# Kernel optimization log

Hardware: AMD Instinct MI355X
Metric: run time of the kernel (lower is better)

## Reference

```python
import jax, jax.numpy as jnp
import numpy as np

INF = 1.0e6
SIGMA = 1.0
RADIUS = 2.5
M, N, H, K, C_IN, C_OUT = 50000, 50000, 32, 15, 128, 128
EXTENT = 10.0  # spatial extent of the random point cloud


def setup_inputs() -> dict:
    key = jax.random.key(0)
    k1, k2, k3, k4, k5, k6 = jax.random.split(key, 6)
    q_pts = jax.random.uniform(k1, (M, 3), dtype=jnp.float32) * EXTENT
    s_pts = jax.random.uniform(k2, (N, 3), dtype=jnp.float32) * EXTENT
    s_feats = jax.random.normal(k3, (N, C_IN), dtype=jnp.float32)
    neighb_inds = jax.random.randint(k4, (M, H), 0, N, dtype=jnp.int64)
    # kernel points: random points inside sphere of given radius (stand-in for load_kernels)
    kp = jax.random.normal(k5, (K, 3), dtype=jnp.float32)
    kp = kp / jnp.linalg.norm(kp, axis=1, keepdims=True) * (RADIUS * 0.66)
    kernel_points = kp.at[0].set(0.0)  # fixed center point
    # kaiming-uniform-like init
    bound = 1.0 / np.sqrt(C_IN)
    weights = jax.random.uniform(k6, (K, C_IN, C_OUT), dtype=jnp.float32,
                                 minval=-bound, maxval=bound)
    return {"q_pts": q_pts, "s_pts": s_pts, "s_feats": s_feats,
            "neighb_inds": neighb_inds, "kernel_points": kernel_points,
            "weights": weights}


def reference(q_pts, s_pts, s_feats, neighb_inds, kernel_points, weights):
    # pad support points with a far-away point so out-of-range indices get zero influence
    s_pts_pad = jnp.concatenate([s_pts, jnp.full((1, 3), INF, s_pts.dtype)], axis=0)
    neighbors = s_pts_pad[neighb_inds] - q_pts[:, None, :]          # (M, H, 3)
    diffs = neighbors[:, :, None, :] - kernel_points[None, None]    # (M, H, K, 3)
    sq_dist = jnp.sum(diffs * diffs, axis=-1)                       # (M, H, K)
    # linear influence, clipped at 0 (no_grad in torch -> stop_gradient here)
    w = jnp.clip(1.0 - jnp.sqrt(sq_dist) / SIGMA, 0.0)              # (M, H, K)
    neighbor_weights = jax.lax.stop_gradient(jnp.swapaxes(w, 1, 2)) # (M, K, H)
    # gather neighbor features (padded with a zero row)
    feats_pad = jnp.concatenate([s_feats, jnp.zeros((1, s_feats.shape[1]), s_feats.dtype)], axis=0)
    neighbor_feats = feats_pad[neighb_inds]                         # (M, H, C_in)
    weighted_feats = jnp.matmul(neighbor_weights, neighbor_feats)   # (M, K, C_in)
    return jnp.einsum('mkc,kcd->md', weighted_feats, weights)       # (M, C_out)
```

## Files before the change

### kernel.cpp

```cpp
#include <hip/hip_runtime.h>

#define M_Q 50000
#define N_S 50000
#define H_N 32
#define K_P 15
#define C_IN 128
#define C_OUT 128

#define G_QB 64
#define G_NT 256
#define NB_GEO ((M_Q + G_QB - 1) / G_QB)
#define LCAP 64

#define WTF_SLOTS (K_P * 8 * 4 * 64)
#define NB_WCVT (WTF_SLOTS / 256)

#define NB_ZERO 1024

#define ENT 128
#define SUBT (ENT / 16)
#define CAPK 12288
#define K2_TILES (CAPK / ENT)

#define WS_CNT_OFF 0
#define WS_WTF_OFF 256
#define WS_WTF_BYTES (WTF_SLOTS * 16)
#define WS_BKT_OFF (WS_WTF_OFF + WS_WTF_BYTES)
#define WS_BKT_BYTES (K_P * CAPK * 8)
#define WS_NEED (WS_BKT_OFF + WS_BKT_BYTES)

typedef __attribute__((ext_vector_type(8))) short s8v;
typedef __attribute__((ext_vector_type(4))) float f4v;
typedef __attribute__((ext_vector_type(4))) float fl4;
typedef __attribute__((ext_vector_type(4))) unsigned u4v;

static __device__ __forceinline__ unsigned f2bf_bits(float x) {
    union { float f; unsigned u; } v; v.f = x;
    return (v.u + 0x7fffu + ((v.u >> 16) & 1u)) >> 16;
}
static __device__ __forceinline__ unsigned pack_bf16(float a, float b) {
    return f2bf_bits(a) | (f2bf_bits(b) << 16);
}

template <typename IT>
__global__ __launch_bounds__(G_NT) void k1_geom(
    const float* __restrict__ q_pts,
    const float* __restrict__ s_pts,
    const IT* __restrict__ inds,
    const float* __restrict__ kp,
    const float* __restrict__ W,
    unsigned* __restrict__ ws_u,
    float* __restrict__ out)
{
    const int b = blockIdx.x;
    const int t = threadIdx.x;

    if (b >= NB_GEO) {
        if (b >= NB_GEO + NB_WCVT) {
            const int zb = b - NB_GEO - NB_WCVT;
            fl4* o4 = (fl4*)out;
            const fl4 z = {0.0f, 0.0f, 0.0f, 0.0f};
            for (int i = zb * G_NT + t; i < M_Q * C_OUT / 4; i += NB_ZERO * G_NT)
                o4[i] = z;
            return;
        }
        const int i = (b - NB_GEO) * 256 + t;
        if (i < WTF_SLOTS) {
            const int lane = i & 63;
            const int kk = (i >> 6) & 3;
            const int col = (i >> 8) & 7;
            const int k = i >> 11;
            const int d = col * 16 + (lane & 15);
            const int c0 = kk * 32 + (lane >> 4) * 8;
            unsigned short* dst =
                (unsigned short*)((char*)ws_u + WS_WTF_OFF) + (size_t)i * 8;
            u4v g;
            unsigned short* gs = (unsigned short*)&g;
            #pragma unroll
            for (int j = 0; j < 8; ++j)
                gs[j] = (unsigned short)f2bf_bits(W[((size_t)k * 128 + c0 + j) * 128 + d]);
            *(u4v*)dst = g;
        }
        return;
    }

    __shared__ float s_kp[K_P * 3];
    __shared__ float s_q[G_QB * 3];
    __shared__ int s_lcnt[K_P];
    __shared__ uint2 s_le[K_P][LCAP];
    __shared__ int s_gb[K_P], s_gc[K_P];

    const int qbase = b * G_QB;
    if (t < K_P * 3) s_kp[t] = kp[t];
    if (t < K_P) s_lcnt[t] = 0;
    if (t < G_QB * 3) {
        int g = qbase * 3 + t;
        s_q[t] = (g < M_Q * 3) ? q_pts[g] : 0.0f;
    }
    __syncthreads();

    #pragma unroll
    for (int it = 0; it < 8; ++it) {
        const int task = it * G_NT + t;
        const int q = task >> 5, h = task & 31;
        const int qg = qbase + q;
        if (qg < M_Q) {
            long long idx = (long long)inds[(size_t)qg * H_N + h];
            if ((unsigned long long)idx < (unsigned long long)N_S) {
                const int i32 = (int)idx;
                const float rx = s_pts[i32 * 3 + 0] - s_q[q * 3 + 0];
                const float ry = s_pts[i32 * 3 + 1] - s_q[q * 3 + 1];
                const float rz = s_pts[i32 * 3 + 2] - s_q[q * 3 + 2];
                #pragma unroll
                for (int k = 0; k < K_P; ++k) {
                    const float dx = rx - s_kp[k * 3 + 0];
                    const float dy = ry - s_kp[k * 3 + 1];
                    const float dz = rz - s_kp[k * 3 + 2];
                    const float d2 = dx * dx + dy * dy + dz * dz;
                    if (d2 < 1.0f) {
                        const float wgt = 1.0f - sqrtf(d2);
                        const int pos = atomicAdd(&s_lcnt[k], 1);
                        if (pos < LCAP)
                            s_le[k][pos] = make_uint2(((unsigned)qg << 16) | (unsigned)i32,
                                                      __float_as_uint(wgt));
                    }
                }
            }
        }
    }
    __syncthreads();

    if (t < K_P) {
        const int cl = min(s_lcnt[t], LCAP);
        const int base = (int)atomicAdd(&ws_u[t], (unsigned)cl);
        s_gb[t] = base;
        const int avail = CAPK - base;
        s_gc[t] = max(0, min(cl, avail));
    }
    __syncthreads();

    uint2* bkt = (uint2*)((char*)ws_u + WS_BKT_OFF);
    #pragma unroll
    for (int k = 0; k < K_P; ++k) {
        if (t < s_gc[k])
            bkt[(size_t)k * CAPK + s_gb[k] + t] = s_le[k][t];
    }
}

__global__ __launch_bounds__(256, 3) void k2_gemm(
    const float* __restrict__ s_feats,
    const unsigned* __restrict__ ws_u,
    float* __restrict__ out)
{
    const int k = blockIdx.x;
    const int base = blockIdx.y * ENT;
    const int cnt = min((int)ws_u[k], CAPK);
    int n_e = cnt - base;
    if (n_e <= 0) return;
    if (n_e > ENT) n_e = ENT;

    __shared__ unsigned short s_A[SUBT * 4 * 64 * 8];
    __shared__ unsigned s_mi[ENT];

    const int t = threadIdx.x;
    const int lane = t & 63;
    const int w = t >> 6;
    const int quad = lane >> 4, l15 = lane & 15;

    const unsigned short* wk =
        (const unsigned short*)((const char*)ws_u + WS_WTF_OFF) + (size_t)k * 2048 * 8;
    s8v bf[2][4];
    #pragma unroll
    for (int nc = 0; nc < 2; ++nc)
        #pragma unroll
        for (int kk = 0; kk < 4; ++kk)
            bf[nc][kk] = *(const s8v*)(wk +
                (size_t)((((w * 2 + nc) * 4) + kk) * 64 + lane) * 8);

    const int e = t >> 1, half = t & 1;
    {
        const int sub = e >> 4, l15e = e & 15;
        if (e < n_e) {
            const uint2* bkt = (const uint2*)((const char*)ws_u + WS_BKT_OFF)
                               + (size_t)k * CAPK + base;
            const uint2 be = bkt[e];
            const unsigned mi = be.x;
            const float wgt = __uint_as_float(be.y);
            if (half == 0) s_mi[e] = mi;
            const float* fr = s_feats + (size_t)(mi & 0xffffu) * C_IN + half * 64;
            #pragma unroll
            for (int j = 0; j < 4; ++j) {
                const fl4 fa = *(const fl4*)(fr + j * 16);
                const fl4 fb = *(const fl4*)(fr + j * 16 + 4);
                const fl4 fc = *(const fl4*)(fr + j * 16 + 8);
                const fl4 fd = *(const fl4*)(fr + j * 16 + 12);
                u4v g0, g1;
                g0[0] = pack_bf16(wgt * fa.x, wgt * fa.y);
                g0[1] = pack_bf16(wgt * fa.z, wgt * fa.w);
                g0[2] = pack_bf16(wgt * fb.x, wgt * fb.y);
                g0[3] = pack_bf16(wgt * fb.z, wgt * fb.w);
                g1[0] = pack_bf16(wgt * fc.x, wgt * fc.y);
                g1[1] = pack_bf16(wgt * fc.z, wgt * fc.w);
                g1[2] = pack_bf16(wgt * fd.x, wgt * fd.y);
                g1[3] = pack_bf16(wgt * fd.z, wgt * fd.w);
                const int cs = half * 64 + j * 16;
                const int kk = cs >> 5;
                const int qd = (cs >> 3) & 3;
                *(u4v*)&s_A[(size_t)(((sub * 4 + kk) * 64) + qd * 16 + l15e) * 8] = g0;
                *(u4v*)&s_A[(size_t)(((sub * 4 + kk) * 64) + (qd + 1) * 16 + l15e) * 8] = g1;
            }
        } else {
            if (half == 0) s_mi[e] = 0xffffffffu;
            const u4v z = {0u, 0u, 0u, 0u};
            #pragma unroll
            for (int j = 0; j < 4; ++j) {
                const int cs = half * 64 + j * 16;
                const int kk = cs >> 5;
                const int qd = (cs >> 3) & 3;
                *(u4v*)&s_A[(size_t)(((sub * 4 + kk) * 64) + qd * 16 + l15e) * 8] = z;
                *(u4v*)&s_A[(size_t)(((sub * 4 + kk) * 64) + (qd + 1) * 16 + l15e) * 8] = z;
            }
        }
    }
    __syncthreads();

    const f4v zf = {0.0f, 0.0f, 0.0f, 0.0f};
    f4v acc[SUBT][2];
    #pragma unroll
    for (int s = 0; s < SUBT; ++s) { acc[s][0] = zf; acc[s][1] = zf; }

    #pragma unroll
    for (int s = 0; s < SUBT; ++s) {
        s8v af[4];
        #pragma unroll
        for (int kk = 0; kk < 4; ++kk)
            af[kk] = *(const s8v*)&s_A[(size_t)((s * 4 + kk) * 64 + lane) * 8];
        #pragma unroll
        for (int nc = 0; nc < 2; ++nc)
            #pragma unroll
            for (int kk = 0; kk < 4; ++kk)
                acc[s][nc] = __builtin_amdgcn_mfma_f32_16x16x32_bf16(
                    af[kk], bf[nc][kk], acc[s][nc], 0, 0, 0);
    }

    #pragma unroll
    for (int s = 0; s < SUBT; ++s) {
        #pragma unroll
        for (int r = 0; r < 4; ++r) {
            const unsigned mi = s_mi[s * 16 + quad * 4 + r];
            const unsigned m = mi >> 16;
            if (m < M_Q) {
                float* op = out + (size_t)m * C_OUT + w * 32 + l15;
                atomicAdd(op,      acc[s][0][r]);
                atomicAdd(op + 16, acc[s][1][r]);
            }
        }
    }
}

template <typename IT>
__global__ __launch_bounds__(128, 8) void kpconv_v1(
    const float* __restrict__ q_pts, const float* __restrict__ s_pts,
    const float* __restrict__ s_feats, const IT* __restrict__ neighb_inds,
    const float* __restrict__ kernel_points, const float* __restrict__ weights,
    float* __restrict__ out)
{
    __shared__ float s_kp[K_P * 3];
    __shared__ float s_w[K_P][H_N];
    __shared__ int s_idx[H_N];
    __shared__ unsigned s_hmask, s_kmask;
    __shared__ float s_wf[K_P][C_IN];
    const int m = blockIdx.x, tid = threadIdx.x;
    if (tid < K_P * 3) s_kp[tid] = kernel_points[tid];
    if (tid == 0) { s_hmask = 0u; s_kmask = 0u; }
    __syncthreads();
    if (tid < H_N) {
        long long idx = (long long)neighb_inds[(size_t)m * H_N + tid];
        const float qx = q_pts[m * 3], qy = q_pts[m * 3 + 1], qz = q_pts[m * 3 + 2];
        float rx, ry, rz; int idx32;
        if ((unsigned long long)idx < (unsigned long long)N_S) {
            idx32 = (int)idx;
            rx = s_pts[idx32 * 3] - qx; ry = s_pts[idx32 * 3 + 1] - qy; rz = s_pts[idx32 * 3 + 2] - qz;
        } else { idx32 = 0; rx = ry = rz = 1.0e6f; }
        s_idx[tid] = idx32;
        unsigned kmask = 0u;
        #pragma unroll
        for (int k = 0; k < K_P; ++k) {
            const float dx = rx - s_kp[k * 3], dy = ry - s_kp[k * 3 + 1], dz = rz - s_kp[k * 3 + 2];
            const float w = fmaxf(1.0f - sqrtf(dx * dx + dy * dy + dz * dz), 0.0f);
            s_w[k][tid] = w;
            if (w > 0.0f) kmask |= (1u << k);
        }
        if (kmask) { atomicOr(&s_hmask, 1u << tid); atomicOr(&s_kmask, kmask); }
    }
    __syncthreads();
    const unsigned hmask = s_hmask, kmask = s_kmask;
    float wf[K_P];
    #pragma unroll
    for (int k = 0; k < K_P; ++k) wf[k] = 0.0f;
    unsigned hmv = hmask;
    while (hmv) {
        const int h = __builtin_ctz(hmv); hmv &= hmv - 1;
        const float f = s_feats[(size_t)s_idx[h] * C_IN + tid];
        #pragma unroll
        for (int k = 0; k < K_P; ++k) wf[k] = fmaf(s_w[k][h], f, wf[k]);
    }
    #pragma unroll
    for (int k = 0; k < K_P; ++k) s_wf[k][tid] = wf[k];
    __syncthreads();
    float a = 0.0f;
    unsigned km = kmask;
    while (km) {
        const int k = __builtin_ctz(km); km &= km - 1;
        const float* Wk = weights + (size_t)k * C_IN * C_OUT + tid;
        #pragma unroll 8
        for (int c = 0; c < C_IN; ++c) a = fmaf(s_wf[k][c], Wk[(size_t)c * C_OUT], a);
    }
    out[(size_t)m * C_OUT + tid] = a;
}

extern "C" void kernel_launch(void* const* d_in, const int* in_sizes, int n_in,
                              void* d_out, int out_size, void* d_ws, size_t ws_size,
                              hipStream_t stream) {
    const float* q_pts         = (const float*)d_in[0];
    const float* s_pts         = (const float*)d_in[1];
    const float* s_feats       = (const float*)d_in[2];
    const float* kernel_points = (const float*)d_in[4];
    const float* weights       = (const float*)d_in[5];
    float* out = (float*)d_out;
    const bool i64 = (in_sizes[3] == 2 * M_Q * H_N);

    if (ws_size < (size_t)WS_NEED) {
        dim3 grid(M_Q), block(128);
        if (i64)
            kpconv_v1<long long><<<grid, block, 0, stream>>>(
                q_pts, s_pts, s_feats, (const long long*)d_in[3], kernel_points, weights, out);
        else
            kpconv_v1<int><<<grid, block, 0, stream>>>(
                q_pts, s_pts, s_feats, (const int*)d_in[3], kernel_points, weights, out);
        return;
    }

    unsigned* ws_u = (unsigned*)d_ws;
    hipMemsetAsync(d_ws, 0, 64, stream);

    dim3 g1(NB_GEO + NB_WCVT + NB_ZERO), b1(G_NT);
    if (i64)
        k1_geom<long long><<<g1, b1, 0, stream>>>(
            q_pts, s_pts, (const long long*)d_in[3], kernel_points, weights, ws_u, out);
    else
        k1_geom<int><<<g1, b1, 0, stream>>>(
            q_pts, s_pts, (const int*)d_in[3], kernel_points, weights, ws_u, out);

    dim3 g2(K_P, K2_TILES), b2(256);
    k2_gemm<<<g2, b2, 0, stream>>>(s_feats, ws_u, out);
}
```

Baseline: 159.1 us.

## Fuse geometry and per-kernel-point MFMA into one kernel with shared-memory accumulation

```diff
diff --git a/kernel.cpp b/kernel.cpp
--- a/kernel.cpp
+++ b/kernel.cpp
@@ -11,23 +11,11 @@
 #define G_NT 256
 #define NB_GEO ((M_Q + G_QB - 1) / G_QB)
 #define LCAP 64
+#define ACC_STRIDE 132
 
 #define WTF_SLOTS (K_P * 8 * 4 * 64)
 #define NB_WCVT (WTF_SLOTS / 256)
-
-#define NB_ZERO 1024
-
-#define ENT 128
-#define SUBT (ENT / 16)
-#define CAPK 12288
-#define K2_TILES (CAPK / ENT)
-
-#define WS_CNT_OFF 0
-#define WS_WTF_OFF 256
-#define WS_WTF_BYTES (WTF_SLOTS * 16)
-#define WS_BKT_OFF (WS_WTF_OFF + WS_WTF_BYTES)
-#define WS_BKT_BYTES (K_P * CAPK * 8)
-#define WS_NEED (WS_BKT_OFF + WS_BKT_BYTES)
+#define WS_NEED (WTF_SLOTS * 16)
 
 typedef __attribute__((ext_vector_type(8))) short s8v;
 typedef __attribute__((ext_vector_type(4))) float f4v;
@@ -42,60 +30,56 @@
     return f2bf_bits(a) | (f2bf_bits(b) << 16);
 }
 
+__global__ __launch_bounds__(256) void k0_wcvt(
+    const float* __restrict__ W, unsigned short* __restrict__ wtf)
+{
+    const int i = blockIdx.x * 256 + threadIdx.x;
+    if (i >= WTF_SLOTS) return;
+    const int lane = i & 63;
+    const int kk = (i >> 6) & 3;
+    const int col = (i >> 8) & 7;
+    const int k = i >> 11;
+    const int d = col * 16 + (lane & 15);
+    const int c0 = kk * 32 + (lane >> 4) * 8;
+    u4v g;
+    unsigned short* gs = (unsigned short*)&g;
+    #pragma unroll
+    for (int j = 0; j < 8; ++j)
+        gs[j] = (unsigned short)f2bf_bits(W[((size_t)k * 128 + c0 + j) * 128 + d]);
+    *(u4v*)(wtf + (size_t)i * 8) = g;
+}
+
 template <typename IT>
-__global__ __launch_bounds__(G_NT) void k1_geom(
+__global__ __launch_bounds__(G_NT, 3) void kpconv_fused(
     const float* __restrict__ q_pts,
     const float* __restrict__ s_pts,
+    const float* __restrict__ s_feats,
     const IT* __restrict__ inds,
     const float* __restrict__ kp,
-    const float* __restrict__ W,
-    unsigned* __restrict__ ws_u,
+    const unsigned short* __restrict__ wtf,
     float* __restrict__ out)
 {
-    const int b = blockIdx.x;
-    const int t = threadIdx.x;
-
-    if (b >= NB_GEO) {
-        if (b >= NB_GEO + NB_WCVT) {
-            const int zb = b - NB_GEO - NB_WCVT;
-            fl4* o4 = (fl4*)out;
-            const fl4 z = {0.0f, 0.0f, 0.0f, 0.0f};
-            for (int i = zb * G_NT + t; i < M_Q * C_OUT / 4; i += NB_ZERO * G_NT)
-                o4[i] = z;
-            return;
-        }
-        const int i = (b - NB_GEO) * 256 + t;
-        if (i < WTF_SLOTS) {
-            const int lane = i & 63;
-            const int kk = (i >> 6) & 3;
-            const int col = (i >> 8) & 7;
-            const int k = i >> 11;
-            const int d = col * 16 + (lane & 15);
-            const int c0 = kk * 32 + (lane >> 4) * 8;
-            unsigned short* dst =
-                (unsigned short*)((char*)ws_u + WS_WTF_OFF) + (size_t)i * 8;
-            u4v g;
-            unsigned short* gs = (unsigned short*)&g;
-            #pragma unroll
-            for (int j = 0; j < 8; ++j)
-                gs[j] = (unsigned short)f2bf_bits(W[((size_t)k * 128 + c0 + j) * 128 + d]);
-            *(u4v*)dst = g;
-        }
-        return;
-    }
-
     __shared__ float s_kp[K_P * 3];
     __shared__ float s_q[G_QB * 3];
     __shared__ int s_lcnt[K_P];
     __shared__ uint2 s_le[K_P][LCAP];
-    __shared__ int s_gb[K_P], s_gc[K_P];
-
+    __shared__ float s_acc[G_QB][ACC_STRIDE];
+
+    const int b = blockIdx.x;
+    const int t = threadIdx.x;
     const int qbase = b * G_QB;
+
     if (t < K_P * 3) s_kp[t] = kp[t];
     if (t < K_P) s_lcnt[t] = 0;
     if (t < G_QB * 3) {
-        int g = qbase * 3 + t;
+        const int g = qbase * 3 + t;
         s_q[t] = (g < M_Q * 3) ? q_pts[g] : 0.0f;
+    }
+    {
+        fl4* a4 = (fl4*)&s_acc[0][0];
+        const fl4 z = {0.0f, 0.0f, 0.0f, 0.0f};
+        #pragma unroll
+        for (int i = t; i < G_QB * ACC_STRIDE / 4; i += G_NT) a4[i] = z;
     }
     __syncthreads();
 
@@ -121,7 +105,7 @@
                         const float wgt = 1.0f - sqrtf(d2);
                         const int pos = atomicAdd(&s_lcnt[k], 1);
                         if (pos < LCAP)
-                            s_le[k][pos] = make_uint2(((unsigned)qg << 16) | (unsigned)i32,
+                            s_le[k][pos] = make_uint2(((unsigned)q << 16) | (unsigned)i32,
                                                       __float_as_uint(wgt));
                     }
                 }
@@ -130,131 +114,63 @@
     }
     __syncthreads();
 
-    if (t < K_P) {
-        const int cl = min(s_lcnt[t], LCAP);
-        const int base = (int)atomicAdd(&ws_u[t], (unsigned)cl);
-        s_gb[t] = base;
-        const int avail = CAPK - base;
-        s_gc[t] = max(0, min(cl, avail));
-    }
-    __syncthreads();
-
-    uint2* bkt = (uint2*)((char*)ws_u + WS_BKT_OFF);
-    #pragma unroll
-    for (int k = 0; k < K_P; ++k) {
-        if (t < s_gc[k])
-            bkt[(size_t)k * CAPK + s_gb[k] + t] = s_le[k][t];
-    }
-}
-
-__global__ __launch_bounds__(256, 3) void k2_gemm(
-    const float* __restrict__ s_feats,
-    const unsigned* __restrict__ ws_u,
-    float* __restrict__ out)
-{
-    const int k = blockIdx.x;
-    const int base = blockIdx.y * ENT;
-    const int cnt = min((int)ws_u[k], CAPK);
-    int n_e = cnt - base;
-    if (n_e <= 0) return;
-    if (n_e > ENT) n_e = ENT;
-
-    __shared__ unsigned short s_A[SUBT * 4 * 64 * 8];
-    __shared__ unsigned s_mi[ENT];
-
-    const int t = threadIdx.x;
     const int lane = t & 63;
     const int w = t >> 6;
     const int quad = lane >> 4, l15 = lane & 15;
 
-    const unsigned short* wk =
-        (const unsigned short*)((const char*)ws_u + WS_WTF_OFF) + (size_t)k * 2048 * 8;
-    s8v bf[2][4];
-    #pragma unroll
-    for (int nc = 0; nc < 2; ++nc)
-        #pragma unroll
-        for (int kk = 0; kk < 4; ++kk)
-            bf[nc][kk] = *(const s8v*)(wk +
-                (size_t)((((w * 2 + nc) * 4) + kk) * 64 + lane) * 8);
-
-    const int e = t >> 1, half = t & 1;
-    {
-        const int sub = e >> 4, l15e = e & 15;
-        if (e < n_e) {
-            const uint2* bkt = (const uint2*)((const char*)ws_u + WS_BKT_OFF)
-                               + (size_t)k * CAPK + base;
-            const uint2 be = bkt[e];
-            const unsigned mi = be.x;
-            const float wgt = __uint_as_float(be.y);
-            if (half == 0) s_mi[e] = mi;
-            const float* fr = s_feats + (size_t)(mi & 0xffffu) * C_IN + half * 64;
+    for (int k = w; k < K_P; k += 4) {
+        const int cnt = min(s_lcnt[k], LCAP);
+        const unsigned short* wk = wtf + (size_t)k * 2048 * 8;
+        for (int sub = 0; sub * 16 < cnt; ++sub) {
+            const int e = sub * 16 + l15;
+            uint2 ent = make_uint2(0u, 0u);
+            if (e < cnt) ent = s_le[k][e];
+            const float wgt = __uint_as_float(ent.y);
+            const float* fr = s_feats + (size_t)(ent.x & 0xffffu) * C_IN + quad * 8;
+            s8v af[4];
             #pragma unroll
-            for (int j = 0; j < 4; ++j) {
-                const fl4 fa = *(const fl4*)(fr + j * 16);
-                const fl4 fb = *(const fl4*)(fr + j * 16 + 4);
-                const fl4 fc = *(const fl4*)(fr + j * 16 + 8);
-                const fl4 fd = *(const fl4*)(fr + j * 16 + 12);
-                u4v g0, g1;
-                g0[0] = pack_bf16(wgt * fa.x, wgt * fa.y);
-                g0[1] = pack_bf16(wgt * fa.z, wgt * fa.w);
-                g0[2] = pack_bf16(wgt * fb.x, wgt * fb.y);
-                g0[3] = pack_bf16(wgt * fb.z, wgt * fb.w);
-                g1[0] = pack_bf16(wgt * fc.x, wgt * fc.y);
-                g1[1] = pack_bf16(wgt * fc.z, wgt * fc.w);
-                g1[2] = pack_bf16(wgt * fd.x, wgt * fd.y);
-                g1[3] = pack_bf16(wgt * fd.z, wgt * fd.w);
-                const int cs = half * 64 + j * 16;
-                const int kk = cs >> 5;
-                const int qd = (cs >> 3) & 3;
-                *(u4v*)&s_A[(size_t)(((sub * 4 + kk) * 64) + qd * 16 + l15e) * 8] = g0;
-                *(u4v*)&s_A[(size_t)(((sub * 4 + kk) * 64) + (qd + 1) * 16 + l15e) * 8] = g1;
-            }
-        } else {
-            if (half == 0) s_mi[e] = 0xffffffffu;
-            const u4v z = {0u, 0u, 0u, 0u};
+            for (int kk = 0; kk < 4; ++kk) {
+                const fl4 a  = *(const fl4*)(fr + kk * 32);
+                const fl4 bb = *(const fl4*)(fr + kk * 32 + 4);
+                u4v g;
+                g[0] = pack_bf16(wgt * a.x,  wgt * a.y);
+                g[1] = pack_bf16(wgt * a.z,  wgt * a.w);
+                g[2] = pack_bf16(wgt * bb.x, wgt * bb.y);
+                g[3] = pack_bf16(wgt * bb.z, wgt * bb.w);
+                af[kk] = *(s8v*)&g;
+            }
+            int m4[4];
             #pragma unroll
-            for (int j = 0; j < 4; ++j) {
-                const int cs = half * 64 + j * 16;
-                const int kk = cs >> 5;
-                const int qd = (cs >> 3) & 3;
-                *(u4v*)&s_A[(size_t)(((sub * 4 + kk) * 64) + qd * 16 + l15e) * 8] = z;
-                *(u4v*)&s_A[(size_t)(((sub * 4 + kk) * 64) + (qd + 1) * 16 + l15e) * 8] = z;
+            for (int r = 0; r < 4; ++r) {
+                const int er = sub * 16 + quad * 4 + r;
+                m4[r] = (er < cnt) ? (int)(s_le[k][er].x >> 16) : -1;
+            }
+            #pragma unroll
+            for (int nc = 0; nc < 8; ++nc) {
+                s8v bfr[4];
+                #pragma unroll
+                for (int kk = 0; kk < 4; ++kk)
+                    bfr[kk] = *(const s8v*)(wk + (size_t)((nc * 4 + kk) * 64 + lane) * 8);
+                f4v acc = {0.0f, 0.0f, 0.0f, 0.0f};
+                #pragma unroll
+                for (int kk = 0; kk < 4; ++kk)
+                    acc = __builtin_amdgcn_mfma_f32_16x16x32_bf16(af[kk], bfr[kk], acc, 0, 0, 0);
+                #pragma unroll
+                for (int r = 0; r < 4; ++r)
+                    if (m4[r] >= 0)
+                        atomicAdd(&s_acc[m4[r]][nc * 16 + l15], acc[r]);
             }
         }
     }
     __syncthreads();
 
-    const f4v zf = {0.0f, 0.0f, 0.0f, 0.0f};
-    f4v acc[SUBT][2];
-    #pragma unroll
-    for (int s = 0; s < SUBT; ++s) { acc[s][0] = zf; acc[s][1] = zf; }
-
-    #pragma unroll
-    for (int s = 0; s < SUBT; ++s) {
-        s8v af[4];
-        #pragma unroll
-        for (int kk = 0; kk < 4; ++kk)
-            af[kk] = *(const s8v*)&s_A[(size_t)((s * 4 + kk) * 64 + lane) * 8];
-        #pragma unroll
-        for (int nc = 0; nc < 2; ++nc)
-            #pragma unroll
-            for (int kk = 0; kk < 4; ++kk)
-                acc[s][nc] = __builtin_amdgcn_mfma_f32_16x16x32_bf16(
-                    af[kk], bf[nc][kk], acc[s][nc], 0, 0, 0);
-    }
-
-    #pragma unroll
-    for (int s = 0; s < SUBT; ++s) {
-        #pragma unroll
-        for (int r = 0; r < 4; ++r) {
-            const unsigned mi = s_mi[s * 16 + quad * 4 + r];
-            const unsigned m = mi >> 16;
-            if (m < M_Q) {
-                float* op = out + (size_t)m * C_OUT + w * 32 + l15;
-                atomicAdd(op,      acc[s][0][r]);
-                atomicAdd(op + 16, acc[s][1][r]);
-            }
-        }
+    const int mmax = min(G_QB, M_Q - qbase);
+    #pragma unroll
+    for (int it = 0; it < 8; ++it) {
+        const int idx = it * G_NT + t;
+        const int row = idx >> 5, c4 = (idx & 31) * 4;
+        if (row < mmax)
+            *(fl4*)(out + (size_t)(qbase + row) * C_OUT + c4) = *(const fl4*)&s_acc[row][c4];
     }
 }
 
@@ -341,17 +257,14 @@
         return;
     }
 
-    unsigned* ws_u = (unsigned*)d_ws;
-    hipMemsetAsync(d_ws, 0, 64, stream);
-
-    dim3 g1(NB_GEO + NB_WCVT + NB_ZERO), b1(G_NT);
+    unsigned short* wtf = (unsigned short*)d_ws;
+    k0_wcvt<<<dim3(NB_WCVT), dim3(256), 0, stream>>>(weights, wtf);
+
+    dim3 g(NB_GEO), bl(G_NT);
     if (i64)
-        k1_geom<long long><<<g1, b1, 0, stream>>>(
-            q_pts, s_pts, (const long long*)d_in[3], kernel_points, weights, ws_u, out);
+        kpconv_fused<long long><<<g, bl, 0, stream>>>(
+            q_pts, s_pts, s_feats, (const long long*)d_in[3], kernel_points, wtf, out);
     else
-        k1_geom<int><<<g1, b1, 0, stream>>>(
-            q_pts, s_pts, (const int*)d_in[3], kernel_points, weights, ws_u, out);
-
-    dim3 g2(K_P, K2_TILES), b2(256);
-    k2_gemm<<<g2, b2, 0, stream>>>(s_feats, ws_u, out);
-}
+        kpconv_fused<int><<<g, bl, 0, stream>>>(
+            q_pts, s_pts, s_feats, (const int*)d_in[3], kernel_points, wtf, out);
+}
```

Measured after the change: 209.2 us. 31.5% more time.
